# Kernel tuning notes

Hardware: AMD Instinct MI355X
Metric: run time of the kernel (lower is better)

Reference implementation:

```python
import jax, jax.numpy as jnp
import numpy as np

NPOINT = 1024
RADIUS = 0.1
NSAMPLE = 32
EPS = 1e-5


def farthest_point_sample(xyz, npoint):
    # xyz: [B, N, 3] -> indices [B, npoint]
    B, N, _ = xyz.shape

    def step(carry, _):
        mind, far = carry  # [B,N], [B]
        centroid = jnp.take_along_axis(xyz, far[:, None, None], axis=1)  # [B,1,3]
        d = jnp.sum((xyz - centroid) ** 2, axis=-1)  # [B,N]
        mind = jnp.minimum(mind, d)
        return (mind, jnp.argmax(mind, axis=-1).astype(jnp.int32)), far

    init = (jnp.full((B, N), 1e10, xyz.dtype), jnp.zeros((B,), jnp.int32))
    _, idx = jax.lax.scan(step, init, None, length=npoint)  # [npoint, B]
    return idx.T


def ball_query(xyz, new_xyz, radius, nsample):
    # xyz [B,N,3], new_xyz [B,S,3] -> neighbor idx [B,S,nsample]
    N = xyz.shape[1]
    d2 = jnp.sum((new_xyz[:, :, None, :] - xyz[:, None, :, :]) ** 2, axis=-1)  # [B,S,N]
    idx = jnp.where(d2 <= radius ** 2, jnp.arange(N, dtype=jnp.int32), N)
    idx = jnp.sort(idx, axis=-1)[..., :nsample]
    first = idx[..., :1]  # center itself is always in-radius, so first is valid
    return jnp.where(idx == N, first, idx)


def _gather(x, idx):
    # x [B,N,C], idx [B,...] -> [B,...,C]
    return jax.vmap(lambda a, i: a[i])(x, idx)


def setup_inputs() -> dict:
    key = jax.random.key(0)
    ks = jax.random.split(key, 8)
    B, N, D = 16, 8192, 64
    inp = {
        "xyz": jax.random.uniform(ks[0], (B, 3, N), jnp.float32),
        "points": jax.random.normal(ks[1], (B, D, N), jnp.float32),
        "w0": jax.random.normal(ks[2], (64, 67), jnp.float32) * 0.05,
        "b0": jnp.zeros((64,), jnp.float32),
        "g0": jnp.ones((64,), jnp.float32),
        "beta0": jnp.zeros((64,), jnp.float32),
        "w1": jax.random.normal(ks[3], (64, 64), jnp.float32) * 0.05,
        "b1": jnp.zeros((64,), jnp.float32),
        "g1": jnp.ones((64,), jnp.float32),
        "beta1": jnp.zeros((64,), jnp.float32),
        "w2": jax.random.normal(ks[4], (128, 64), jnp.float32) * 0.05,
        "b2": jnp.zeros((128,), jnp.float32),
        "g2": jnp.ones((128,), jnp.float32),
        "beta2": jnp.zeros((128,), jnp.float32),
    }
    return inp


def reference(xyz, points, w0, b0, g0, beta0, w1, b1, g1, beta1, w2, b2, g2, beta2):
    # xyz [B,3,N], points [B,D,N]
    xyz_t = jnp.transpose(xyz, (0, 2, 1))      # [B,N,3]
    pts_t = jnp.transpose(points, (0, 2, 1))   # [B,N,D]

    fps_idx = farthest_point_sample(xyz_t, NPOINT)          # [B,S]
    new_xyz = _gather(xyz_t, fps_idx)                        # [B,S,3]
    gidx = ball_query(xyz_t, new_xyz, RADIUS, NSAMPLE)       # [B,S,K]

    grouped_xyz = _gather(xyz_t, gidx) - new_xyz[:, :, None, :]  # [B,S,K,3]
    grouped_pts = _gather(pts_t, gidx)                           # [B,S,K,D]
    feat = jnp.concatenate([grouped_xyz, grouped_pts], axis=-1)  # [B,S,K,3+D]
    B, S, K, C = feat.shape
    new_points = jnp.transpose(feat.reshape(B, S * K, C), (0, 2, 1))  # [B,C,S*K]

    for w, b, g, be in ((w0, b0, g0, beta0), (w1, b1, g1, beta1), (w2, b2, g2, beta2)):
        x = jnp.einsum('bcl,oc->bol', new_points, w) + b[None, :, None]
        mean = x.mean(axis=(0, 2), keepdims=True)
        var = x.var(axis=(0, 2), keepdims=True)
        new_points = jax.nn.relu(g[None, :, None] * (x - mean)
                                 * jax.lax.rsqrt(var + EPS) + be[None, :, None])

    new_points = jnp.max(new_points, axis=2)  # [B, mlp[-1]]
    return jnp.transpose(new_xyz, (0, 2, 1)), new_points
```

## Files before the change

### kernel.cpp

```cpp
#include <hip/hip_runtime.h>
#include <stdint.h>
#include <limits.h>

__device__ inline float mul_rn(float a, float b){ float r; asm("v_mul_f32 %0, %1, %2" : "=v"(r) : "v"(a), "v"(b)); return r; }
__device__ inline float add_rn(float a, float b){ float r; asm("v_add_f32 %0, %1, %2" : "=v"(r) : "v"(a), "v"(b)); return r; }
__device__ inline float sub_rn(float a, float b){ float r; asm("v_sub_f32 %0, %1, %2" : "=v"(r) : "v"(a), "v"(b)); return r; }

typedef uint16_t u16x8 __attribute__((ext_vector_type(8)));
typedef float    f32x2 __attribute__((ext_vector_type(2)));

__device__ inline float bf2f(uint16_t u){ return __uint_as_float(((uint32_t)u) << 16); }
__device__ inline uint16_t f2bf(float f){
    uint32_t u = __float_as_uint(f);
    u += 0x7fffu + ((u >> 16) & 1u);
    return (uint16_t)(u >> 16);
}
__device__ inline unsigned fkey(float f){
    unsigned u = __float_as_uint(f);
    return (u & 0x80000000u) ? ~u : (u | 0x80000000u);
}
__device__ inline float funkey(unsigned k){
    unsigned u = (k & 0x80000000u) ? (k ^ 0x80000000u) : ~k;
    return __uint_as_float(u);
}

__device__ inline unsigned dpp_umax_wave(unsigned v){
    unsigned t;
    t = (unsigned)__builtin_amdgcn_update_dpp((int)v, (int)v, 0x111, 0xf, 0xf, false); v = v > t ? v : t;
    t = (unsigned)__builtin_amdgcn_update_dpp((int)v, (int)v, 0x112, 0xf, 0xf, false); v = v > t ? v : t;
    t = (unsigned)__builtin_amdgcn_update_dpp((int)v, (int)v, 0x114, 0xf, 0xf, false); v = v > t ? v : t;
    t = (unsigned)__builtin_amdgcn_update_dpp((int)v, (int)v, 0x118, 0xf, 0xf, false); v = v > t ? v : t;
    t = (unsigned)__builtin_amdgcn_update_dpp((int)v, (int)v, 0x142, 0xf, 0xf, false); v = v > t ? v : t;
    t = (unsigned)__builtin_amdgcn_update_dpp((int)v, (int)v, 0x143, 0xf, 0xf, false); v = v > t ? v : t;
    return v;
}

#define NPTS   8192
#define NBATCH 16
#define NPOINT 1024
#define NSAMP  32
#define LCOLS  32768
#define NTOT   524288.0f
#define NBUCK  32

#define OFF_FPS   0u
#define OFF_GIDX  65536u
#define OFF_SSC   2162688u
#define OFF_MM    2263040u
#define OFF_WT    2279424u
#define OFF_T0    4194304u
#define OFF_T1    71303168u
#define OFF_PTST  138412032u

__global__ __launch_bounds__(512) void fps_fused_kernel(const float* __restrict__ xyz,
        int* __restrict__ fps_idx, float* __restrict__ out_xyz,
        const float* __restrict__ pts, uint16_t* __restrict__ ptsT,
        const float* __restrict__ w0, const float* __restrict__ w1, const float* __restrict__ w2,
        float* __restrict__ wt0, float* __restrict__ wt1, float* __restrict__ wt2){
#pragma clang fp contract(off)
    __shared__ __align__(16) float smem[33824];
    const int bid = blockIdx.x, tid = threadIdx.x;

    if (bid >= 2064){
        int t = (bid - 2064) * 512 + tid;
        if (t < 64*67){ int o = t / 67, c = t % 67; wt0[c*64 + o] = w0[t]; }
        if (t < 64*64){ int o = t >> 6, c = t & 63; wt1[c*64 + o] = w1[t]; }
        if (t < 128*64){ int o = t >> 6, c = t & 63; wt2[c*128 + o] = w2[t]; }
        return;
    }
    if (bid >= 16){
        float (*tile)[65] = (float(*)[65])smem;
        const int tb = bid - 16;
        const int bt = tb >> 7, n0 = (tb & 127) << 6;
        const int tn = tid & 63, tg = tid >> 6;
        const float* src = pts + (size_t)bt * 64 * NPTS + n0;
#pragma unroll
        for (int i = 0; i < 8; i++){ int c = tg*8 + i; tile[c][tn] = src[(size_t)c * NPTS + tn]; }
        __syncthreads();
        uint16_t* dst = ptsT + ((size_t)bt * NPTS + n0) * 64;
#pragma unroll
        for (int i = 0; i < 8; i++){ int n = tg*8 + i; dst[(size_t)n * 64 + tn] = f2bf(tile[tn][n]); }
        return;
    }

    float* sxyz = smem;
    float4* sxyz4 = (float4*)smem;
    unsigned long long* wslots = (unsigned long long*)(smem + 32768);
    int* sidx = (int*)(smem + 32800);
    const int b = bid;
    const float* px = xyz + (size_t)b * 3 * NPTS;
    for (int i = tid; i < NPTS; i += 512)
        sxyz4[i] = float4{px[i], px[NPTS + i], px[2*NPTS + i], 0.f};
    __syncthreads();

    const int p0 = tid << 4;
    const float4* rp = sxyz4 + p0;
    f32x2 X2[8], Y2[8], Z2[8], M2[8];
#pragma unroll
    for (int j = 0; j < 8; j++){
        float4 qa = rp[2*j], qb = rp[2*j + 1];
        X2[j] = f32x2{qa.x, qb.x};
        Y2[j] = f32x2{qa.y, qb.y};
        Z2[j] = f32x2{qa.z, qb.z};
        M2[j] = f32x2{1e10f, 1e10f};
    }
    const unsigned base = ~(unsigned)p0;

    int cur = 0;
    float cx = sxyz[0], cy = sxyz[1], cz = sxyz[2];
    for (int t = 0; t < NPOINT; t++){
        if (tid == 0) sidx[t] = cur;
        const f32x2 c2x = f32x2{cx, cx}, c2y = f32x2{cy, cy}, c2z = f32x2{cz, cz};
#pragma unroll
        for (int j = 0; j < 8; j++){
            f32x2 dx = X2[j] - c2x;
            f32x2 dy = Y2[j] - c2y;
            f32x2 dz = Z2[j] - c2z;
            f32x2 d2 = dx*dx + dy*dy + dz*dz;
            M2[j].x = fminf(M2[j].x, d2.x);
            M2[j].y = fminf(M2[j].y, d2.y);
        }
        float tv[8];
#pragma unroll
        for (int j = 0; j < 8; j++) tv[j] = fmaxf(M2[j].x, M2[j].y);
        float t0_ = fmaxf(fmaxf(tv[0], tv[1]), fmaxf(tv[2], tv[3]));
        float t1_ = fmaxf(fmaxf(tv[4], tv[5]), fmaxf(tv[6], tv[7]));
        const float mt = fmaxf(t0_, t1_);
        unsigned jpos = 0;
#pragma unroll
        for (int j = 7; j >= 0; j--){
            if (M2[j].y == mt) jpos = 2*j + 1;
            if (M2[j].x == mt) jpos = 2*j;
        }
        const unsigned lo = base - jpos;
        const unsigned mtu = __float_as_uint(mt);
        unsigned vm = dpp_umax_wave(mtu);
        const unsigned wvu = __builtin_amdgcn_readlane(vm, 63);
        unsigned long long cand = __ballot(mtu == wvu);
        const int fl = __ffsll((long long)cand) - 1;
        const unsigned wlo = __builtin_amdgcn_readlane(lo, fl);
        if ((tid & 63) == 0)
            wslots[(t & 1) * 8 + (tid >> 6)] = (((unsigned long long)wvu) << 32) | wlo;
        __syncthreads();
        const ulonglong2* sp = (const ulonglong2*)(wslots + (t & 1) * 8);
        ulonglong2 ka = sp[0], kb = sp[1], kc = sp[2], kd = sp[3];
        unsigned long long ma = (ka.y > ka.x) ? ka.y : ka.x;
        unsigned long long mb = (kb.y > kb.x) ? kb.y : kb.x;
        unsigned long long mc = (kc.y > kc.x) ? kc.y : kc.x;
        unsigned long long md = (kd.y > kd.x) ? kd.y : kd.x;
        unsigned long long mab = (mb > ma) ? mb : ma;
        unsigned long long mcd = (md > mc) ? md : mc;
        unsigned long long win = (mcd > mab) ? mcd : mab;
        cur = (int)(~((unsigned)win));
        const float4 cc4 = sxyz4[cur];
        cx = cc4.x; cy = cc4.y; cz = cc4.z;
    }
    __syncthreads();
#pragma unroll
    for (int q = 0; q < 2; q++){
        const int i = (q << 9) + tid;
        const int idx = sidx[i];
        fps_idx[b * NPOINT + i] = idx;
        const float4 c4 = sxyz4[idx];
        float* oxp = out_xyz + b * 3 * NPOINT;
        oxp[i]            = c4.x;
        oxp[NPOINT + i]   = c4.y;
        oxp[2*NPOINT + i] = c4.z;
    }
}

__global__ __launch_bounds__(256) void ballquery_kernel(const float* __restrict__ xyz,
                                                        const int* __restrict__ fps_idx, int* __restrict__ gidx){
    const int w = (blockIdx.x << 2) + (threadIdx.x >> 6);
    const int lane = threadIdx.x & 63;
    const int b = w >> 10, s = w & 1023;
    const float* px = xyz + (size_t)b * 3 * NPTS;
    const int ci = fps_idx[b * NPOINT + s];
    const float cx = px[ci], cy = px[NPTS+ci], cz = px[2*NPTS+ci];
    int* gout = gidx + (size_t)b * LCOLS + s * NSAMP;
    int have = 0, first_p = 0; bool got = false;
    for (int c0 = 0; c0 < NPTS; c0 += 64){
        int p = c0 + lane;
        float dx = sub_rn(px[p], cx), dy = sub_rn(px[NPTS+p], cy), dz = sub_rn(px[2*NPTS+p], cz);
        float d2 = add_rn(add_rn(mul_rn(dx,dx), mul_rn(dy,dy)), mul_rn(dz,dz));
        bool in = (d2 <= 0.01f);
        unsigned long long m = __ballot(in);
        if (m && !got){ first_p = c0 + __ffsll(m) - 1; got = true; }
        if (in){
            int pos = have + __popcll(m & ((1ull << lane) - 1ull));
            if (pos < NSAMP) gout[pos] = p;
        }
        have += __popcll(m);
        if (have >= NSAMP) break;
    }
    for (int pos = have + lane; pos < NSAMP; pos += 64) gout[pos] = first_p;
}

template<int CIN, int COUT, bool ACT, bool GATHER, bool WRITE, bool MAXMIN>
__global__ __launch_bounds__(256) void mm_kernel(const uint16_t* __restrict__ xin,
        const float* __restrict__ xyz, const float* __restrict__ nx,
        const uint16_t* __restrict__ ptsT, const int* __restrict__ gidx,
        const float* __restrict__ wt, const float* __restrict__ bias,
        const float* __restrict__ pssc, const float* __restrict__ pg, const float* __restrict__ pbeta,
        uint16_t* __restrict__ xout, float* __restrict__ ssc,
        unsigned* __restrict__ mmax, unsigned* __restrict__ mmin){
    __shared__ __align__(16) float sw[CIN * COUT];
    __shared__ float sb[COUT];
    __shared__ float sa[ACT ? 2*CIN : 1];
    __shared__ __align__(16) float sred[16 * 260];
    const int tid = threadIdx.x;
    for (int i = tid; i < CIN * COUT; i += 256) sw[i] = wt[i];
    if (tid < COUT) sb[tid] = bias[tid];
    if constexpr (ACT){
        if (tid < CIN){
            float s = 0.f, ss = 0.f;
#pragma unroll 4
            for (int k = 0; k < NBUCK; k++){ s += pssc[k*256 + tid]; ss += pssc[k*256 + 128 + tid]; }
            const float inv = 1.0f / NTOT;
            float mean = s * inv;
            float var  = ss * inv - mean * mean;
            float a = pg[tid] / sqrtf(var + 1e-5f);
            sa[tid] = a;
            sa[CIN + tid] = fmaf(-mean, a, pbeta[tid]);
        }
    }
    __syncthreads();
    const int b = blockIdx.x >> 7;
    const int ls = ((blockIdx.x & 127) << 8) + tid;
    float f[CIN];
    if constexpr (GATHER){
        const int s = ls >> 5;
        const int g = gidx[(size_t)b * LCOLS + ls];
        const float* px = xyz + (size_t)b * 3 * NPTS;
        const float cx = nx[b*3*NPOINT + s], cy = nx[b*3*NPOINT + NPOINT + s], cz = nx[b*3*NPOINT + 2*NPOINT + s];
        f[0] = sub_rn(px[g], cx); f[1] = sub_rn(px[NPTS+g], cy); f[2] = sub_rn(px[2*NPTS+g], cz);
        const u16x8* pr = (const u16x8*)(ptsT + ((size_t)b * NPTS + (size_t)g) * 64);
#pragma unroll
        for (int jj = 0; jj < 8; jj++){
            u16x8 v = pr[jj];
#pragma unroll
            for (int e = 0; e < 8; e++) f[3 + jj*8 + e] = bf2f(v[e]);
        }
    } else {
        const uint16_t* xp = xin + (size_t)b * CIN * LCOLS + ls;
#pragma unroll
        for (int c = 0; c < CIN; c++){
            float v = bf2f(xp[(size_t)c * LCOLS]);
            if constexpr (ACT) v = fmaxf(fmaf(sa[c], v, sa[CIN + c]), 0.0f);
            f[c] = v;
        }
    }
    uint16_t* op = xout + (size_t)b * COUT * LCOLS + ls;
    float* sbck = ssc + (blockIdx.x & (NBUCK-1)) * 256;
    for (int o0 = 0; o0 < COUT; o0 += 16){
        float acc[16];
#pragma unroll
        for (int j = 0; j < 16; j++) acc[j] = sb[o0 + j];
#pragma unroll
        for (int c = 0; c < CIN; c++){
            const float4* wr = (const float4*)(sw + c * COUT + o0);
            float4 w0_ = wr[0], w1_ = wr[1], w2_ = wr[2], w3_ = wr[3];
            const float fc = f[c];
            acc[0]  = fmaf(w0_.x, fc, acc[0]);  acc[1]  = fmaf(w0_.y, fc, acc[1]);
            acc[2]  = fmaf(w0_.z, fc, acc[2]);  acc[3]  = fmaf(w0_.w, fc, acc[3]);
            acc[4]  = fmaf(w1_.x, fc, acc[4]);  acc[5]  = fmaf(w1_.y, fc, acc[5]);
            acc[6]  = fmaf(w1_.z, fc, acc[6]);  acc[7]  = fmaf(w1_.w, fc, acc[7]);
            acc[8]  = fmaf(w2_.x, fc, acc[8]);  acc[9]  = fmaf(w2_.y, fc, acc[9]);
            acc[10] = fmaf(w2_.z, fc, acc[10]); acc[11] = fmaf(w2_.w, fc, acc[11]);
            acc[12] = fmaf(w3_.x, fc, acc[12]); acc[13] = fmaf(w3_.y, fc, acc[13]);
            acc[14] = fmaf(w3_.z, fc, acc[14]); acc[15] = fmaf(w3_.w, fc, acc[15]);
        }
        if constexpr (WRITE){
#pragma unroll
            for (int j = 0; j < 16; j++) op[(size_t)(o0 + j) * LCOLS] = f2bf(acc[j]);
        }
        __syncthreads();
#pragma unroll
        for (int k = 0; k < 16; k++) sred[k * 260 + tid] = acc[k];
        __syncthreads();
        const int ch = tid >> 4, seg = tid & 15;
        float s = 0.f, ss = 0.f, mx = -1e30f, mn = 1e30f;
        const float4* rp = (const float4*)(sred + ch * 260 + seg * 16);
#pragma unroll
        for (int e = 0; e < 4; e++){
            float4 v = rp[e];
            s += v.x + v.y + v.z + v.w;
            ss = fmaf(v.x, v.x, ss); ss = fmaf(v.y, v.y, ss);
            ss = fmaf(v.z, v.z, ss); ss = fmaf(v.w, v.w, ss);
            if constexpr (MAXMIN){
                mx = fmaxf(mx, fmaxf(fmaxf(v.x, v.y), fmaxf(v.z, v.w)));
                mn = fminf(mn, fminf(fminf(v.x, v.y), fminf(v.z, v.w)));
            }
        }
#pragma unroll
        for (int off = 1; off < 16; off <<= 1){
            s += __shfl_xor(s, off); ss += __shfl_xor(ss, off);
            if constexpr (MAXMIN){ mx = fmaxf(mx, __shfl_xor(mx, off)); mn = fminf(mn, __shfl_xor(mn, off)); }
        }
        if (seg == 0){
            atomicAdd(&sbck[o0 + ch], s);
            atomicAdd(&sbck[128 + o0 + ch], ss);
            if constexpr (MAXMIN){
                atomicMax(&mmax[b * 128 + o0 + ch], fkey(mx));
                atomicMin(&mmin[b * 128 + o0 + ch], fkey(mn));
            }
        }
    }
}

__global__ __launch_bounds__(64) void final_kernel(const float* __restrict__ ssc, const float* __restrict__ g2,
                                                   const float* __restrict__ be2, const unsigned* __restrict__ mmax,
                                                   const unsigned* __restrict__ mmin, float* __restrict__ out){
    const int t = blockIdx.x * 64 + threadIdx.x;
    const int o = t & 127;
    float s = 0.f, ss = 0.f;
    for (int k = 0; k < NBUCK; k++){ s += ssc[k*256 + o]; ss += ssc[k*256 + 128 + o]; }
    const float inv = 1.0f / NTOT;
    float mean = s * inv;
    float var  = ss * inv - mean * mean;
    float a = g2[o] / sqrtf(var + 1e-5f);
    float c = fmaf(-mean, a, be2[o]);
    unsigned k = (a >= 0.f) ? mmax[t] : mmin[t];
    float x = funkey(k);
    out[49152 + t] = fmaxf(fmaf(a, x, c), 0.0f);
}

extern "C" void kernel_launch(void* const* d_in, const int* in_sizes, int n_in,
                              void* d_out, int out_size, void* d_ws, size_t ws_size,
                              hipStream_t stream){
    const float* xyz = (const float*)d_in[0];
    const float* pts = (const float*)d_in[1];
    const float* w0  = (const float*)d_in[2];  const float* b0  = (const float*)d_in[3];
    const float* g0  = (const float*)d_in[4];  const float* be0 = (const float*)d_in[5];
    const float* w1  = (const float*)d_in[6];  const float* b1  = (const float*)d_in[7];
    const float* g1  = (const float*)d_in[8];  const float* be1 = (const float*)d_in[9];
    const float* w2  = (const float*)d_in[10]; const float* b2  = (const float*)d_in[11];
    const float* g2  = (const float*)d_in[12]; const float* be2 = (const float*)d_in[13];
    float* out = (float*)d_out;
    char* ws = (char*)d_ws;

    int*      fps_idx = (int*)(ws + OFF_FPS);
    int*      gidx    = (int*)(ws + OFF_GIDX);
    float*    ssc0    = (float*)(ws + OFF_SSC);
    float*    ssc1    = ssc0 + NBUCK*256;
    float*    ssc2    = ssc1 + NBUCK*256;
    unsigned* mmax    = (unsigned*)(ws + OFF_MM);
    unsigned* mmin    = mmax + 2048;
    float*    wt0     = (float*)(ws + OFF_WT);
    float*    wt1     = wt0 + 67*64;
    float*    wt2     = wt1 + 64*64;
    uint16_t* t0      = (uint16_t*)(ws + OFF_T0);
    uint16_t* t1      = (uint16_t*)(ws + OFF_T1);
    uint16_t* ptsT    = (uint16_t*)(ws + OFF_PTST);

    hipMemsetAsync(ws + OFF_SSC, 0, 3 * NBUCK * 256 * 4, stream);
    hipMemsetAsync(ws + OFF_MM, 0x00, 8192, stream);
    hipMemsetAsync(ws + OFF_MM + 8192, 0xFF, 8192, stream);

    fps_fused_kernel<<<2080, 512, 0, stream>>>(xyz, fps_idx, out, pts, ptsT,
                                               w0, w1, w2, wt0, wt1, wt2);
    ballquery_kernel<<<4096, 256, 0, stream>>>(xyz, fps_idx, gidx);

    mm_kernel<67, 64, false, true, true, false><<<2048, 256, 0, stream>>>(
        nullptr, xyz, out, ptsT, gidx, wt0, b0, nullptr, nullptr, nullptr, t0, ssc0, nullptr, nullptr);

    mm_kernel<64, 64, true, false, true, false><<<2048, 256, 0, stream>>>(
        t0, nullptr, nullptr, nullptr, nullptr, wt1, b1, ssc0, g0, be0, t1, ssc1, nullptr, nullptr);

    mm_kernel<64, 128, true, false, false, true><<<2048, 256, 0, stream>>>(
        t1, nullptr, nullptr, nullptr, nullptr, wt2, b2, ssc1, g1, be1, nullptr, ssc2, mmax, mmin);

    final_kernel<<<32, 64, 0, stream>>>(ssc2, g2, be2, mmax, mmin, out);
}
```

Before: 1.342 ms.

## Use bf16 MFMA for the second and third pointwise MLP layers

```diff
diff --git a/kernel.cpp b/kernel.cpp
--- a/kernel.cpp
+++ b/kernel.cpp
@@ -8,6 +8,8 @@
 
 typedef uint16_t u16x8 __attribute__((ext_vector_type(8)));
 typedef float    f32x2 __attribute__((ext_vector_type(2)));
+typedef short    bf16x8 __attribute__((ext_vector_type(8)));
+typedef float    fx4 __attribute__((ext_vector_type(4)));
 
 __device__ inline float bf2f(uint16_t u){ return __uint_as_float(((uint32_t)u) << 16); }
 __device__ inline uint16_t f2bf(float f){
@@ -48,6 +50,8 @@
 #define OFF_SSC   2162688u
 #define OFF_MM    2263040u
 #define OFF_WT    2279424u
+#define OFF_WPK1  2345728u
+#define OFF_WPK2  2353920u
 #define OFF_T0    4194304u
 #define OFF_T1    71303168u
 #define OFF_PTST  138412032u
@@ -56,7 +60,7 @@
         int* __restrict__ fps_idx, float* __restrict__ out_xyz,
         const float* __restrict__ pts, uint16_t* __restrict__ ptsT,
         const float* __restrict__ w0, const float* __restrict__ w1, const float* __restrict__ w2,
-        float* __restrict__ wt0, float* __restrict__ wt1, float* __restrict__ wt2){
+        float* __restrict__ wt0, uint16_t* __restrict__ wpk1, uint16_t* __restrict__ wpk2){
 #pragma clang fp contract(off)
     __shared__ __align__(16) float smem[33824];
     const int bid = blockIdx.x, tid = threadIdx.x;
@@ -64,8 +68,8 @@
     if (bid >= 2064){
         int t = (bid - 2064) * 512 + tid;
         if (t < 64*67){ int o = t / 67, c = t % 67; wt0[c*64 + o] = w0[t]; }
-        if (t < 64*64){ int o = t >> 6, c = t & 63; wt1[c*64 + o] = w1[t]; }
-        if (t < 128*64){ int o = t >> 6, c = t & 63; wt2[c*128 + o] = w2[t]; }
+        if (t < 64*64){ int o = t >> 6, c = t & 63; wpk1[((c>>3)*64  + o)*8 + (c&7)] = f2bf(w1[t]); }
+        if (t < 128*64){ int o = t >> 6, c = t & 63; wpk2[((c>>3)*128 + o)*8 + (c&7)] = f2bf(w2[t]); }
         return;
     }
     if (bid >= 16){
@@ -196,39 +200,22 @@
     for (int pos = have + lane; pos < NSAMP; pos += 64) gout[pos] = first_p;
 }
 
-template<int CIN, int COUT, bool ACT, bool GATHER, bool WRITE, bool MAXMIN>
-__global__ __launch_bounds__(256) void mm_kernel(const uint16_t* __restrict__ xin,
+__global__ __launch_bounds__(256) void mm0_kernel(
         const float* __restrict__ xyz, const float* __restrict__ nx,
         const uint16_t* __restrict__ ptsT, const int* __restrict__ gidx,
         const float* __restrict__ wt, const float* __restrict__ bias,
-        const float* __restrict__ pssc, const float* __restrict__ pg, const float* __restrict__ pbeta,
-        uint16_t* __restrict__ xout, float* __restrict__ ssc,
-        unsigned* __restrict__ mmax, unsigned* __restrict__ mmin){
-    __shared__ __align__(16) float sw[CIN * COUT];
-    __shared__ float sb[COUT];
-    __shared__ float sa[ACT ? 2*CIN : 1];
+        uint16_t* __restrict__ xout, float* __restrict__ ssc){
+    __shared__ __align__(16) float sw[67 * 64];
+    __shared__ float sb[64];
     __shared__ __align__(16) float sred[16 * 260];
     const int tid = threadIdx.x;
-    for (int i = tid; i < CIN * COUT; i += 256) sw[i] = wt[i];
-    if (tid < COUT) sb[tid] = bias[tid];
-    if constexpr (ACT){
-        if (tid < CIN){
-            float s = 0.f, ss = 0.f;
-#pragma unroll 4
-            for (int k = 0; k < NBUCK; k++){ s += pssc[k*256 + tid]; ss += pssc[k*256 + 128 + tid]; }
-            const float inv = 1.0f / NTOT;
-            float mean = s * inv;
-            float var  = ss * inv - mean * mean;
-            float a = pg[tid] / sqrtf(var + 1e-5f);
-            sa[tid] = a;
-            sa[CIN + tid] = fmaf(-mean, a, pbeta[tid]);
-        }
-    }
+    for (int i = tid; i < 67 * 64; i += 256) sw[i] = wt[i];
+    if (tid < 64) sb[tid] = bias[tid];
     __syncthreads();
     const int b = blockIdx.x >> 7;
     const int ls = ((blockIdx.x & 127) << 8) + tid;
-    float f[CIN];
-    if constexpr (GATHER){
+    float f[67];
+    {
         const int s = ls >> 5;
         const int g = gidx[(size_t)b * LCOLS + ls];
         const float* px = xyz + (size_t)b * 3 * NPTS;
@@ -241,24 +228,16 @@
 #pragma unroll
             for (int e = 0; e < 8; e++) f[3 + jj*8 + e] = bf2f(v[e]);
         }
-    } else {
-        const uint16_t* xp = xin + (size_t)b * CIN * LCOLS + ls;
-#pragma unroll
-        for (int c = 0; c < CIN; c++){
-            float v = bf2f(xp[(size_t)c * LCOLS]);
-            if constexpr (ACT) v = fmaxf(fmaf(sa[c], v, sa[CIN + c]), 0.0f);
-            f[c] = v;
-        }
-    }
-    uint16_t* op = xout + (size_t)b * COUT * LCOLS + ls;
+    }
+    uint16_t* op = xout + (size_t)b * 64 * LCOLS + ls;
     float* sbck = ssc + (blockIdx.x & (NBUCK-1)) * 256;
-    for (int o0 = 0; o0 < COUT; o0 += 16){
+    for (int o0 = 0; o0 < 64; o0 += 16){
         float acc[16];
 #pragma unroll
         for (int j = 0; j < 16; j++) acc[j] = sb[o0 + j];
 #pragma unroll
-        for (int c = 0; c < CIN; c++){
-            const float4* wr = (const float4*)(sw + c * COUT + o0);
+        for (int c = 0; c < 67; c++){
+            const float4* wr = (const float4*)(sw + c * 64 + o0);
             float4 w0_ = wr[0], w1_ = wr[1], w2_ = wr[2], w3_ = wr[3];
             const float fc = f[c];
             acc[0]  = fmaf(w0_.x, fc, acc[0]);  acc[1]  = fmaf(w0_.y, fc, acc[1]);
@@ -270,16 +249,14 @@
             acc[12] = fmaf(w3_.x, fc, acc[12]); acc[13] = fmaf(w3_.y, fc, acc[13]);
             acc[14] = fmaf(w3_.z, fc, acc[14]); acc[15] = fmaf(w3_.w, fc, acc[15]);
         }
-        if constexpr (WRITE){
-#pragma unroll
-            for (int j = 0; j < 16; j++) op[(size_t)(o0 + j) * LCOLS] = f2bf(acc[j]);
-        }
+#pragma unroll
+        for (int j = 0; j < 16; j++) op[(size_t)(o0 + j) * LCOLS] = f2bf(acc[j]);
         __syncthreads();
 #pragma unroll
         for (int k = 0; k < 16; k++) sred[k * 260 + tid] = acc[k];
         __syncthreads();
         const int ch = tid >> 4, seg = tid & 15;
-        float s = 0.f, ss = 0.f, mx = -1e30f, mn = 1e30f;
+        float s = 0.f, ss = 0.f;
         const float4* rp = (const float4*)(sred + ch * 260 + seg * 16);
 #pragma unroll
         for (int e = 0; e < 4; e++){
@@ -287,23 +264,129 @@
             s += v.x + v.y + v.z + v.w;
             ss = fmaf(v.x, v.x, ss); ss = fmaf(v.y, v.y, ss);
             ss = fmaf(v.z, v.z, ss); ss = fmaf(v.w, v.w, ss);
-            if constexpr (MAXMIN){
-                mx = fmaxf(mx, fmaxf(fmaxf(v.x, v.y), fmaxf(v.z, v.w)));
-                mn = fminf(mn, fminf(fminf(v.x, v.y), fminf(v.z, v.w)));
-            }
         }
 #pragma unroll
         for (int off = 1; off < 16; off <<= 1){
             s += __shfl_xor(s, off); ss += __shfl_xor(ss, off);
-            if constexpr (MAXMIN){ mx = fmaxf(mx, __shfl_xor(mx, off)); mn = fminf(mn, __shfl_xor(mn, off)); }
         }
         if (seg == 0){
             atomicAdd(&sbck[o0 + ch], s);
             atomicAdd(&sbck[128 + o0 + ch], ss);
+        }
+    }
+}
+
+template<int COUT, bool WRITE, bool MAXMIN>
+__global__ __launch_bounds__(256) void mfma_mm_kernel(
+        const uint16_t* __restrict__ xin, const uint16_t* __restrict__ wpack,
+        const float* __restrict__ bias,
+        const float* __restrict__ pssc, const float* __restrict__ pg, const float* __restrict__ pbeta,
+        uint16_t* __restrict__ xout, float* __restrict__ ssc,
+        unsigned* __restrict__ mmax, unsigned* __restrict__ mmin){
+    constexpr int MT = COUT / 16;
+    __shared__ __align__(16) uint16_t sB[8 * 256 * 8];
+    __shared__ __align__(16) uint16_t sA[8 * COUT * 8];
+    __shared__ float sa_[64], sc_[64], sb_[COUT];
+    __shared__ float sred_s[4][COUT], sred_ss[4][COUT];
+    __shared__ float sred_mx[MAXMIN ? 4 : 1][COUT], sred_mn[MAXMIN ? 4 : 1][COUT];
+    const int tid = threadIdx.x;
+    const int b = blockIdx.x >> 7;
+    const int n0 = (blockIdx.x & 127) << 8;
+
+    if (tid < 64){
+        float s = 0.f, ss = 0.f;
+#pragma unroll 4
+        for (int k = 0; k < NBUCK; k++){ s += pssc[k*256 + tid]; ss += pssc[k*256 + 128 + tid]; }
+        const float inv = 1.0f / NTOT;
+        float mean = s * inv;
+        float var  = ss * inv - mean * mean;
+        float a = pg[tid] / sqrtf(var + 1e-5f);
+        sa_[tid] = a;
+        sc_[tid] = fmaf(-mean, a, pbeta[tid]);
+    }
+    if (tid < COUT) sb_[tid] = bias[tid];
+    for (int i = tid; i < COUT * 64; i += 256) sA[i] = wpack[i];
+    __syncthreads();
+
+    {
+        const uint16_t* xp = xin + (size_t)b * 64 * LCOLS + (n0 + tid);
+#pragma unroll 8
+        for (int c = 0; c < 64; c++){
+            float v = bf2f(xp[(size_t)c * LCOLS]);
+            v = fmaxf(fmaf(sa_[c], v, sc_[c]), 0.0f);
+            sB[((c >> 3) * 256 + tid) * 8 + (c & 7)] = f2bf(v);
+        }
+    }
+    __syncthreads();
+
+    const int lane = tid & 63, w = tid >> 6;
+    const int lhi = lane >> 4, llo = lane & 15;
+    fx4 acc[MT][4];
+#pragma unroll
+    for (int mt = 0; mt < MT; mt++)
+#pragma unroll
+        for (int nt = 0; nt < 4; nt++) acc[mt][nt] = fx4{0.f, 0.f, 0.f, 0.f};
+
+#pragma unroll
+    for (int kk = 0; kk < 2; kk++){
+        bf16x8 bfrag[4];
+#pragma unroll
+        for (int nt = 0; nt < 4; nt++){
+            int n = w * 64 + nt * 16 + llo;
+            bfrag[nt] = *(const bf16x8*)&sB[((kk*4 + lhi) * 256 + n) * 8];
+        }
+#pragma unroll
+        for (int mt = 0; mt < MT; mt++){
+            bf16x8 afrag = *(const bf16x8*)&sA[((kk*4 + lhi) * COUT + mt*16 + llo) * 8];
+#pragma unroll
+            for (int nt = 0; nt < 4; nt++)
+                acc[mt][nt] = __builtin_amdgcn_mfma_f32_16x16x32_bf16(afrag, bfrag[nt], acc[mt][nt], 0, 0, 0);
+        }
+    }
+
+#pragma unroll
+    for (int mt = 0; mt < MT; mt++){
+#pragma unroll
+        for (int j = 0; j < 4; j++){
+            const int ch = mt*16 + lhi*4 + j;
+            const float bv = sb_[ch];
+            float a0 = acc[mt][0][j] + bv, a1 = acc[mt][1][j] + bv;
+            float a2 = acc[mt][2][j] + bv, a3 = acc[mt][3][j] + bv;
+            acc[mt][0][j] = a0; acc[mt][1][j] = a1; acc[mt][2][j] = a2; acc[mt][3][j] = a3;
+            if constexpr (WRITE){
+                uint16_t* op = xout + (size_t)b * COUT * LCOLS + (size_t)ch * LCOLS + n0 + w*64 + llo;
+                op[0]  = f2bf(a0); op[16] = f2bf(a1); op[32] = f2bf(a2); op[48] = f2bf(a3);
+            }
+            float s  = (a0 + a1) + (a2 + a3);
+            float ss = fmaf(a0, a0, fmaf(a1, a1, fmaf(a2, a2, a3*a3)));
+            float mx = 0.f, mn = 0.f;
             if constexpr (MAXMIN){
-                atomicMax(&mmax[b * 128 + o0 + ch], fkey(mx));
-                atomicMin(&mmin[b * 128 + o0 + ch], fkey(mn));
+                mx = fmaxf(fmaxf(a0, a1), fmaxf(a2, a3));
+                mn = fminf(fminf(a0, a1), fminf(a2, a3));
             }
+#pragma unroll
+            for (int off = 1; off < 16; off <<= 1){
+                s += __shfl_xor(s, off); ss += __shfl_xor(ss, off);
+                if constexpr (MAXMIN){ mx = fmaxf(mx, __shfl_xor(mx, off)); mn = fminf(mn, __shfl_xor(mn, off)); }
+            }
+            if (llo == 0){
+                sred_s[w][ch] = s; sred_ss[w][ch] = ss;
+                if constexpr (MAXMIN){ sred_mx[w][ch] = mx; sred_mn[w][ch] = mn; }
+            }
+        }
+    }
+    __syncthreads();
+    if (tid < COUT){
+        float s  = sred_s[0][tid]  + sred_s[1][tid]  + sred_s[2][tid]  + sred_s[3][tid];
+        float ss = sred_ss[0][tid] + sred_ss[1][tid] + sred_ss[2][tid] + sred_ss[3][tid];
+        float* sbck = ssc + (blockIdx.x & (NBUCK-1)) * 256;
+        atomicAdd(&sbck[tid], s);
+        atomicAdd(&sbck[128 + tid], ss);
+        if constexpr (MAXMIN){
+            float mx = fmaxf(fmaxf(sred_mx[0][tid], sred_mx[1][tid]), fmaxf(sred_mx[2][tid], sred_mx[3][tid]));
+            float mn = fminf(fminf(sred_mn[0][tid], sred_mn[1][tid]), fminf(sred_mn[2][tid], sred_mn[3][tid]));
+            atomicMax(&mmax[b * 128 + tid], fkey(mx));
+            atomicMin(&mmin[b * 128 + tid], fkey(mn));
         }
     }
 }
@@ -347,8 +430,8 @@
     unsigned* mmax    = (unsigned*)(ws + OFF_MM);
     unsigned* mmin    = mmax + 2048;
     float*    wt0     = (float*)(ws + OFF_WT);
-    float*    wt1     = wt0 + 67*64;
-    float*    wt2     = wt1 + 64*64;
+    uint16_t* wpk1    = (uint16_t*)(ws + OFF_WPK1);
+    uint16_t* wpk2    = (uint16_t*)(ws + OFF_WPK2);
     uint16_t* t0      = (uint16_t*)(ws + OFF_T0);
     uint16_t* t1      = (uint16_t*)(ws + OFF_T1);
     uint16_t* ptsT    = (uint16_t*)(ws + OFF_PTST);
@@ -358,17 +441,16 @@
     hipMemsetAsync(ws + OFF_MM + 8192, 0xFF, 8192, stream);
 
     fps_fused_kernel<<<2080, 512, 0, stream>>>(xyz, fps_idx, out, pts, ptsT,
-                                               w0, w1, w2, wt0, wt1, wt2);
+                                               w0, w1, w2, wt0, wpk1, wpk2);
     ballquery_kernel<<<4096, 256, 0, stream>>>(xyz, fps_idx, gidx);
 
-    mm_kernel<67, 64, false, true, true, false><<<2048, 256, 0, stream>>>(
-        nullptr, xyz, out, ptsT, gidx, wt0, b0, nullptr, nullptr, nullptr, t0, ssc0, nullptr, nullptr);
-
-    mm_kernel<64, 64, true, false, true, false><<<2048, 256, 0, stream>>>(
-        t0, nullptr, nullptr, nullptr, nullptr, wt1, b1, ssc0, g0, be0, t1, ssc1, nullptr, nullptr);
-
-    mm_kernel<64, 128, true, false, false, true><<<2048, 256, 0, stream>>>(
-        t1, nullptr, nullptr, nullptr, nullptr, wt2, b2, ssc1, g1, be1, nullptr, ssc2, mmax, mmin);
+    mm0_kernel<<<2048, 256, 0, stream>>>(xyz, out, ptsT, gidx, wt0, b0, t0, ssc0);
+
+    mfma_mm_kernel<64, true, false><<<2048, 256, 0, stream>>>(
+        t0, wpk1, b1, ssc0, g0, be0, t1, ssc1, nullptr, nullptr);
+
+    mfma_mm_kernel<128, false, true><<<2048, 256, 0, stream>>>(
+        t1, wpk2, b2, ssc1, g1, be1, nullptr, ssc2, mmax, mmin);
 
     final_kernel<<<32, 64, 0, stream>>>(ssc2, g2, be2, mmax, mmin, out);
 }
```

Result: faster. 1.214 ms (-9.5%).
